# Performance work log

Measured on AMD Instinct MI355X. Metric: run time of the kernel, lower is better.

The kernel has to match this reference:

```python
import jax, jax.numpy as jnp
from jax import lax
import numpy as np

SIGMA = 1.0
TRUNCATE = 3.0

def _gaussian_1d(sigma, truncate):
    tail = int(sigma * truncate)
    x = np.arange(-tail, tail + 1, dtype=np.float32)
    k = np.exp(-0.5 * x * x / (sigma * sigma))
    k = k / k.sum()
    return jnp.asarray(k, dtype=jnp.float32)  # length 2*tail+1 (=7)


def setup_inputs() -> dict:
    key = jax.random.key(0)
    image = jax.random.normal(key, (2, 160, 160, 160, 4), dtype=jnp.float32)
    return {"image": image}


def reference(image):
    # Separable per-channel (depthwise) Gaussian blur along each spatial axis,
    # SAME padding, stride 1 -- identical math to the TF per-channel conv loop.
    k = _gaussian_1d(SIGMA, TRUNCATE)
    K = k.shape[0]
    C = image.shape[-1]
    out = image
    for d in range(3):  # spatial axes D, H, W
        kshape = [1, 1, 1]
        kshape[d] = K
        # depthwise kernel: (kd, kh, kw, in_per_group=1, C)
        rhs = jnp.broadcast_to(k.reshape(kshape + [1, 1]), tuple(kshape) + (1, C))
        out = lax.conv_general_dilated(
            out, rhs,
            window_strides=(1, 1, 1),
            padding='SAME',
            dimension_numbers=('NDHWC', 'DHWIO', 'NDHWC'),
            feature_group_count=C,
        )
    return out
```

## Files before the change

### kernel.cpp

```cpp
#include <hip/hip_runtime.h>


#define THT 16
#define TWT 16
#define CHUNK 16
#define NS (CHUNK + 6)
#define DIM 160
#define SLICE (DIM * DIM)
#define HALON (22 * 22)
#define NBLK 500

#define W0 0.004433048f
#define W1 0.054005582f
#define W2 0.242036229f
#define W3 0.399050300f

__device__ __forceinline__ float4 blur7(float4 a0, float4 a1, float4 a2, float4 a3,
                                        float4 a4, float4 a5, float4 a6) {
    float4 r;
    r.x = W0 * (a0.x + a6.x) + W1 * (a1.x + a5.x) + W2 * (a2.x + a4.x) + W3 * a3.x;
    r.y = W0 * (a0.y + a6.y) + W1 * (a1.y + a5.y) + W2 * (a2.y + a4.y) + W3 * a3.y;
    r.z = W0 * (a0.z + a6.z) + W1 * (a1.z + a5.z) + W2 * (a2.z + a4.z) + W3 * a3.z;
    r.w = W0 * (a0.w + a6.w) + W1 * (a1.w + a5.w) + W2 * (a2.w + a4.w) + W3 * a3.w;
    return r;
}

__global__ __launch_bounds__(256, 2)
void gauss3d_fused(const float4* __restrict__ in, float4* __restrict__ out) {
    const int bid = blockIdx.x;
    const int xcd = bid & 7;
    const int bix = bid >> 3;
    const int swz = (xcd < 4 ? xcd * 63 : 252 + (xcd - 4) * 62) + bix;

    const int tid  = threadIdx.x;
    const int wv   = tid >> 6;
    const int lane = tid & 63;

    int wid = swz * 4 + wv;
    const int tw    = wid % 10;  wid /= 10;
    const int th    = wid % 10;  wid /= 10;
    const int chunk = wid % 10;  wid /= 10;
    const int n     = wid;

    const int h0 = th * THT;
    const int w0 = tw * TWT;
    const int d0 = chunk * CHUNK;

    __shared__ float4 raw[4][22][23];
    __shared__ float4 wb[4][22][17];
    float4 (* const rawW)[23] = raw[wv];
    float4 (* const wbW)[17]  = wb[wv];

    const size_t nbase = (size_t)n * DIM * SLICE;
    const float4 z = make_float4(0.f, 0.f, 0.f, 0.f);

    int  soff[8], ridx[8];
    bool sok[8];
    #pragma unroll
    for (int s = 0; s < 8; ++s) {
        const int j = lane + 64 * s;
        const bool has = (j < HALON);
        const int rr = has ? (j / 22) : 0, cc = has ? (j % 22) : 0;
        const int gh = h0 + rr - 3, gw = w0 + cc - 3;
        const bool ok = has && gh >= 0 && gh < DIM && gw >= 0 && gw < DIM;
        soff[s] = ok ? (gh * DIM + gw) : 0;
        sok[s]  = ok;
        ridx[s] = rr * 23 + cc;
    }
    const bool has7 = (lane + 448 < HALON);

    const int g1r = lane >> 2, g1c = (lane & 3) * 4;
    const bool hasG2 = (lane < 24);
    const int g2r = (64 + lane) >> 2, g2c = ((64 + lane) & 3) * 4;

    const int q  = lane >> 4;
    const int lw = lane & 15;

    float4 qa0=z,qa1=z,qa2=z,qa3=z,qa4=z,qa5=z,qa6=z;
    float4 qb0=z,qb1=z,qb2=z,qb3=z,qb4=z,qb5=z,qb6=z;
    float4 qc0=z,qc1=z,qc2=z,qc3=z,qc4=z,qc5=z,qc6=z;
    float4 qd0=z,qd1=z,qd2=z,qd3=z,qd4=z,qd5=z,qd6=z;

    float4 pA0, pA1, pA2, pA3, pA4, pA5, pA6, pA7;
    float4 pB0, pB1, pB2, pB3, pB4, pB5, pB6, pB7;

#define PREF(P0,P1,P2,P3,P4,P5,P6,P7, DSL)                                   \
    do {                                                                     \
        const int _d = (DSL);                                                \
        const bool _inr = (_d >= 0) && (_d < DIM);                           \
        const float4* _s = in + nbase + (size_t)(_inr ? _d : 0) * SLICE;     \
        P0 = (_inr && sok[0]) ? _s[soff[0]] : z;                             \
        P1 = (_inr && sok[1]) ? _s[soff[1]] : z;                             \
        P2 = (_inr && sok[2]) ? _s[soff[2]] : z;                             \
        P3 = (_inr && sok[3]) ? _s[soff[3]] : z;                             \
        P4 = (_inr && sok[4]) ? _s[soff[4]] : z;                             \
        P5 = (_inr && sok[5]) ? _s[soff[5]] : z;                             \
        P6 = (_inr && sok[6]) ? _s[soff[6]] : z;                             \
        P7 = (_inr && sok[7]) ? _s[soff[7]] : z;                             \
    } while (0)

#define COMMIT(P0,P1,P2,P3,P4,P5,P6,P7)                                      \
    do {                                                                     \
        float4* rb = &rawW[0][0];                                            \
        rb[ridx[0]] = P0;                                                    \
        rb[ridx[1]] = P1;                                                    \
        rb[ridx[2]] = P2;                                                    \
        rb[ridx[3]] = P3;                                                    \
        rb[ridx[4]] = P4;                                                    \
        rb[ridx[5]] = P5;                                                    \
        rb[ridx[6]] = P6;                                                    \
        if (has7) rb[ridx[7]] = P7;                                          \
    } while (0)

#define WGRP(R, C0)                                                          \
    do {                                                                     \
        const float4* _rr = &rawW[R][0];                                     \
        float4 v0 = _rr[(C0) + 0];                                           \
        float4 v1 = _rr[(C0) + 1];                                           \
        float4 v2 = _rr[(C0) + 2];                                           \
        float4 v3 = _rr[(C0) + 3];                                           \
        float4 v4 = _rr[(C0) + 4];                                           \
        float4 v5 = _rr[(C0) + 5];                                           \
        float4 v6 = _rr[(C0) + 6];                                           \
        float4 v7 = _rr[(C0) + 7];                                           \
        float4 v8 = _rr[(C0) + 8];                                           \
        float4 v9 = _rr[(C0) + 9];                                           \
        float4* _wr = &wbW[R][0];                                            \
        _wr[(C0) + 0] = blur7(v0, v1, v2, v3, v4, v5, v6);                   \
        _wr[(C0) + 1] = blur7(v1, v2, v3, v4, v5, v6, v7);                   \
        _wr[(C0) + 2] = blur7(v2, v3, v4, v5, v6, v7, v8);                   \
        _wr[(C0) + 3] = blur7(v3, v4, v5, v6, v7, v8, v9);                   \
    } while (0)

#define HPHASE(K)                                                            \
    do {                                                                     \
        float4 t0 = wbW[4 * q + 0][lw];                                      \
        float4 t1 = wbW[4 * q + 1][lw];                                      \
        float4 t2 = wbW[4 * q + 2][lw];                                      \
        float4 t3 = wbW[4 * q + 3][lw];                                      \
        float4 t4 = wbW[4 * q + 4][lw];                                      \
        float4 t5 = wbW[4 * q + 5][lw];                                      \
        float4 t6 = wbW[4 * q + 6][lw];                                      \
        float4 t7 = wbW[4 * q + 7][lw];                                      \
        float4 t8 = wbW[4 * q + 8][lw];                                      \
        float4 t9 = wbW[4 * q + 9][lw];                                      \
        float4 va = blur7(t0, t1, t2, t3, t4, t5, t6);                       \
        float4 vb = blur7(t1, t2, t3, t4, t5, t6, t7);                       \
        float4 vc = blur7(t2, t3, t4, t5, t6, t7, t8);                       \
        float4 vd = blur7(t3, t4, t5, t6, t7, t8, t9);                       \
        qa0=qa1; qa1=qa2; qa2=qa3; qa3=qa4; qa4=qa5; qa5=qa6; qa6=va;        \
        qb0=qb1; qb1=qb2; qb2=qb3; qb3=qb4; qb4=qb5; qb5=qb6; qb6=vb;        \
        qc0=qc1; qc1=qc2; qc2=qc3; qc3=qc4; qc4=qc5; qc5=qc6; qc6=vc;        \
        qd0=qd1; qd1=qd2; qd2=qd3; qd3=qd4; qd4=qd5; qd5=qd6; qd6=vd;        \
        if ((K) >= 6) {                                                      \
            const int dout = d0 + (K) - 6;                                   \
            float4 oa = blur7(qa0, qa1, qa2, qa3, qa4, qa5, qa6);            \
            float4 ob = blur7(qb0, qb1, qb2, qb3, qb4, qb5, qb6);            \
            float4 oc = blur7(qc0, qc1, qc2, qc3, qc4, qc5, qc6);            \
            float4 od = blur7(qd0, qd1, qd2, qd3, qd4, qd5, qd6);            \
            const size_t base = nbase + (size_t)dout * SLICE                 \
                              + (size_t)(h0 + 4 * q) * DIM + (w0 + lw);      \
            out[base + 0 * DIM] = oa;                                        \
            out[base + 1 * DIM] = ob;                                        \
            out[base + 2 * DIM] = oc;                                        \
            out[base + 3 * DIM] = od;                                        \
        }                                                                    \
    } while (0)

    PREF(pA0,pA1,pA2,pA3,pA4,pA5,pA6,pA7, d0 - 3);
    PREF(pB0,pB1,pB2,pB3,pB4,pB5,pB6,pB7, d0 - 2);

    for (int k2 = 0; k2 < NS; k2 += 2) {
        {
            COMMIT(pA0,pA1,pA2,pA3,pA4,pA5,pA6,pA7);
            if (k2 + 2 < NS) PREF(pA0,pA1,pA2,pA3,pA4,pA5,pA6,pA7, d0 - 3 + k2 + 2);
            WGRP(g1r, g1c);
            if (hasG2) WGRP(g2r, g2c);
            HPHASE(k2);
        }
        {
            COMMIT(pB0,pB1,pB2,pB3,pB4,pB5,pB6,pB7);
            if (k2 + 3 < NS) PREF(pB0,pB1,pB2,pB3,pB4,pB5,pB6,pB7, d0 - 3 + k2 + 3);
            WGRP(g1r, g1c);
            if (hasG2) WGRP(g2r, g2c);
            HPHASE(k2 + 1);
        }
    }
#undef PREF
#undef COMMIT
#undef WGRP
#undef HPHASE
}

extern "C" void kernel_launch(void* const* d_in, const int* in_sizes, int n_in,
                              void* d_out, int out_size, void* d_ws, size_t ws_size,
                              hipStream_t stream) {
    const float4* in = (const float4*)d_in[0];
    float4* out = (float4*)d_out;
    gauss3d_fused<<<NBLK, 256, 0, stream>>>(in, out);
}
```

Measured before the change: 82.53 us.

## Launch one wave per block and double-buffer LDS slices per wave

Each 256-thread block holding four independent waves becomes a 64-thread single-wave block, with four times as many blocks and a simpler XCD-strided block mapping. Each wave now has separate raw and W-blurred LDS buffers for the A and B depth slices. Both slices are committed, both prefetches issued, then both W passes and both H/D passes run, grouping LDS work into larger batches. LDS per block is about 24 KB, which may limit occupancy, and launch_bounds(64,1) gives the compiler looser register limits.

```diff
diff --git a/kernel.cpp b/kernel.cpp
--- a/kernel.cpp
+++ b/kernel.cpp
@@ -8,7 +8,7 @@
 #define DIM 160
 #define SLICE (DIM * DIM)
 #define HALON (22 * 22)
-#define NBLK 500
+#define NBLK 2000
 
 #define W0 0.004433048f
 #define W1 0.054005582f
@@ -25,18 +25,13 @@
     return r;
 }
 
-__global__ __launch_bounds__(256, 2)
+__global__ __launch_bounds__(64, 1)
 void gauss3d_fused(const float4* __restrict__ in, float4* __restrict__ out) {
     const int bid = blockIdx.x;
-    const int xcd = bid & 7;
-    const int bix = bid >> 3;
-    const int swz = (xcd < 4 ? xcd * 63 : 252 + (xcd - 4) * 62) + bix;
+    int wid = (bid & 7) * (NBLK / 8) + (bid >> 3);
 
-    const int tid  = threadIdx.x;
-    const int wv   = tid >> 6;
-    const int lane = tid & 63;
+    const int lane = threadIdx.x;
 
-    int wid = swz * 4 + wv;
     const int tw    = wid % 10;  wid /= 10;
     const int th    = wid % 10;  wid /= 10;
     const int chunk = wid % 10;  wid /= 10;
@@ -46,10 +41,10 @@
     const int w0 = tw * TWT;
     const int d0 = chunk * CHUNK;
 
-    __shared__ float4 raw[4][22][23];
-    __shared__ float4 wb[4][22][17];
-    float4 (* const rawW)[23] = raw[wv];
-    float4 (* const wbW)[17]  = wb[wv];
+    __shared__ float4 rawA[22][23];
+    __shared__ float4 rawB[22][23];
+    __shared__ float4 wbA[22][17];
+    __shared__ float4 wbB[22][17];
 
     const size_t nbase = (size_t)n * DIM * SLICE;
     const float4 z = make_float4(0.f, 0.f, 0.f, 0.f);
@@ -81,8 +76,8 @@
     float4 qc0=z,qc1=z,qc2=z,qc3=z,qc4=z,qc5=z,qc6=z;
     float4 qd0=z,qd1=z,qd2=z,qd3=z,qd4=z,qd5=z,qd6=z;
 
-    float4 pA0, pA1, pA2, pA3, pA4, pA5, pA6, pA7;
-    float4 pB0, pB1, pB2, pB3, pB4, pB5, pB6, pB7;
+    float4 pA0,pA1,pA2,pA3,pA4,pA5,pA6,pA7;
+    float4 pB0,pB1,pB2,pB3,pB4,pB5,pB6,pB7;
 
 #define PREF(P0,P1,P2,P3,P4,P5,P6,P7, DSL)                                   \
     do {                                                                     \
@@ -99,9 +94,9 @@
         P7 = (_inr && sok[7]) ? _s[soff[7]] : z;                             \
     } while (0)
 
-#define COMMIT(P0,P1,P2,P3,P4,P5,P6,P7)                                      \
+#define COMMIT(RAW, P0,P1,P2,P3,P4,P5,P6,P7)                                 \
     do {                                                                     \
-        float4* rb = &rawW[0][0];                                            \
+        float4* rb = &RAW[0][0];                                             \
         rb[ridx[0]] = P0;                                                    \
         rb[ridx[1]] = P1;                                                    \
         rb[ridx[2]] = P2;                                                    \
@@ -112,9 +107,9 @@
         if (has7) rb[ridx[7]] = P7;                                          \
     } while (0)
 
-#define WGRP(R, C0)                                                          \
+#define WGRP(RAW, WB, R, C0)                                                 \
     do {                                                                     \
-        const float4* _rr = &rawW[R][0];                                     \
+        const float4* _rr = &RAW[R][0];                                      \
         float4 v0 = _rr[(C0) + 0];                                           \
         float4 v1 = _rr[(C0) + 1];                                           \
         float4 v2 = _rr[(C0) + 2];                                           \
@@ -125,25 +120,25 @@
         float4 v7 = _rr[(C0) + 7];                                           \
         float4 v8 = _rr[(C0) + 8];                                           \
         float4 v9 = _rr[(C0) + 9];                                           \
-        float4* _wr = &wbW[R][0];                                            \
+        float4* _wr = &WB[R][0];                                             \
         _wr[(C0) + 0] = blur7(v0, v1, v2, v3, v4, v5, v6);                   \
         _wr[(C0) + 1] = blur7(v1, v2, v3, v4, v5, v6, v7);                   \
         _wr[(C0) + 2] = blur7(v2, v3, v4, v5, v6, v7, v8);                   \
         _wr[(C0) + 3] = blur7(v3, v4, v5, v6, v7, v8, v9);                   \
     } while (0)
 
-#define HPHASE(K)                                                            \
+#define HPHASE(WB, K)                                                        \
     do {                                                                     \
-        float4 t0 = wbW[4 * q + 0][lw];                                      \
-        float4 t1 = wbW[4 * q + 1][lw];                                      \
-        float4 t2 = wbW[4 * q + 2][lw];                                      \
-        float4 t3 = wbW[4 * q + 3][lw];                                      \
-        float4 t4 = wbW[4 * q + 4][lw];                                      \
-        float4 t5 = wbW[4 * q + 5][lw];                                      \
-        float4 t6 = wbW[4 * q + 6][lw];                                      \
-        float4 t7 = wbW[4 * q + 7][lw];                                      \
-        float4 t8 = wbW[4 * q + 8][lw];                                      \
-        float4 t9 = wbW[4 * q + 9][lw];                                      \
+        float4 t0 = WB[4 * q + 0][lw];                                       \
+        float4 t1 = WB[4 * q + 1][lw];                                       \
+        float4 t2 = WB[4 * q + 2][lw];                                       \
+        float4 t3 = WB[4 * q + 3][lw];                                       \
+        float4 t4 = WB[4 * q + 4][lw];                                       \
+        float4 t5 = WB[4 * q + 5][lw];                                       \
+        float4 t6 = WB[4 * q + 6][lw];                                       \
+        float4 t7 = WB[4 * q + 7][lw];                                       \
+        float4 t8 = WB[4 * q + 8][lw];                                       \
+        float4 t9 = WB[4 * q + 9][lw];                                       \
         float4 va = blur7(t0, t1, t2, t3, t4, t5, t6);                       \
         float4 vb = blur7(t1, t2, t3, t4, t5, t6, t7);                       \
         float4 vc = blur7(t2, t3, t4, t5, t6, t7, t8);                       \
@@ -171,20 +166,21 @@
     PREF(pB0,pB1,pB2,pB3,pB4,pB5,pB6,pB7, d0 - 2);
 
     for (int k2 = 0; k2 < NS; k2 += 2) {
-        {
-            COMMIT(pA0,pA1,pA2,pA3,pA4,pA5,pA6,pA7);
-            if (k2 + 2 < NS) PREF(pA0,pA1,pA2,pA3,pA4,pA5,pA6,pA7, d0 - 3 + k2 + 2);
-            WGRP(g1r, g1c);
-            if (hasG2) WGRP(g2r, g2c);
-            HPHASE(k2);
-        }
-        {
-            COMMIT(pB0,pB1,pB2,pB3,pB4,pB5,pB6,pB7);
-            if (k2 + 3 < NS) PREF(pB0,pB1,pB2,pB3,pB4,pB5,pB6,pB7, d0 - 3 + k2 + 3);
-            WGRP(g1r, g1c);
-            if (hasG2) WGRP(g2r, g2c);
-            HPHASE(k2 + 1);
-        }
+        const int din = d0 - 3 + k2;
+
+        COMMIT(rawA, pA0,pA1,pA2,pA3,pA4,pA5,pA6,pA7);
+        COMMIT(rawB, pB0,pB1,pB2,pB3,pB4,pB5,pB6,pB7);
+
+        if (k2 + 2 < NS) PREF(pA0,pA1,pA2,pA3,pA4,pA5,pA6,pA7, din + 2);
+        if (k2 + 3 < NS) PREF(pB0,pB1,pB2,pB3,pB4,pB5,pB6,pB7, din + 3);
+
+        WGRP(rawA, wbA, g1r, g1c);
+        if (hasG2) WGRP(rawA, wbA, g2r, g2c);
+        WGRP(rawB, wbB, g1r, g1c);
+        if (hasG2) WGRP(rawB, wbB, g2r, g2c);
+
+        HPHASE(wbA, k2);
+        HPHASE(wbB, k2 + 1);
     }
 #undef PREF
 #undef COMMIT
@@ -197,5 +193,5 @@
                               hipStream_t stream) {
     const float4* in = (const float4*)d_in[0];
     float4* out = (float4*)d_out;
-    gauss3d_fused<<<NBLK, 256, 0, stream>>>(in, out);
+    gauss3d_fused<<<NBLK, 64, 0, stream>>>(in, out);
 }
```

Measured after the change: 86.91 us, median of 2. 5.3% more time.
